# Kernel tuning notes

Hardware: AMD Instinct MI355X
Metric: run time of the kernel (lower is better)

## Reference

```python
import jax, jax.numpy as jnp
import numpy as np

DT = 0.02          # matches sdeint(dt=0.02)
N_STEPS = 50       # (times[-1]-times[0]) / DT with times = linspace(0, 1, 50)


def lipswish(x):
    # LipSwish activation: 0.909 * x * sigmoid(x)
    return 0.909 * x * jax.nn.sigmoid(x)


def mlp(y, ws, bs):
    # ws: [L, H, H], bs: [L, H]; LipSwish between layers, linear output
    L = ws.shape[0]
    for i in range(L):
        y = y @ ws[i] + bs[i]
        if i < L - 1:
            y = lipswish(y)
    return y


def setup_inputs() -> dict:
    key = jax.random.key(0)
    ks = jax.random.split(key, 12)
    B, T, D, H, FH, L = 1024, 50, 64, 1024, 128, 2

    def lin(k, fan_in, shape):
        return (jax.random.normal(k, shape, jnp.float32) / np.sqrt(fan_in)).astype(jnp.float32)

    return {
        "coeffs": jax.random.normal(ks[0], (B, T, D), jnp.float32),
        "times": jnp.linspace(0.0, 1.0, T).astype(jnp.float32),
        "dw": jax.random.normal(ks[1], (N_STEPS, B, H), jnp.float32),  # std-normal; scaled by sqrt(DT) inside
        # vector field: drift f and diagonal diffusion g, each a 2-layer MLP H->H
        "f_ws": lin(ks[2], H, (L, H, H)),
        "f_bs": jnp.zeros((L, H), jnp.float32),
        "g_ws": lin(ks[3], H, (L, H, H)),
        "g_bs": jnp.zeros((L, H), jnp.float32),
        # decoder / embedding layers
        "initial_w": lin(ks[4], D, (D, H)),
        "initial_b": jnp.zeros((H,), jnp.float32),
        "lin_in_w": lin(ks[5], H, (H, FH)),
        "lin_in_b": jnp.zeros((FH,), jnp.float32),
        "emb_w": lin(ks[6], 2 * FH, (2 * FH, H)),
        "emb_b": jnp.zeros((H,), jnp.float32),
        "samp_w": lin(ks[7], H, (H, FH)),
        "samp_b": jnp.zeros((FH,), jnp.float32),
    }


def reference(coeffs, times, dw, f_ws, f_bs, g_ws, g_bs,
              initial_w, initial_b, lin_in_w, lin_in_b,
              emb_w, emb_b, samp_w, samp_b):
    B = coeffs.shape[0]
    FH = samp_w.shape[1]

    # X.evaluate(times) at the interpolation knots == coeffs; take first time point
    y0 = (coeffs @ initial_w + initial_b)[:, 0, :]  # [B, H]

    sqrt_dt = jnp.asarray(np.sqrt(DT), y0.dtype)

    # Euler-Maruyama: y_{k+1} = y_k + f(t,y)*dt + g(t,y)*dW_k  (diagonal noise)
    def step(y, dwk):
        drift = mlp(y, f_ws, f_bs)
        diff = mlp(y, g_ws, g_bs)
        y = y + drift * DT + diff * (dwk * sqrt_dt)
        return y, None

    z, _ = jax.lax.scan(step, y0, dw)  # z: [B, H] (z_t[-1])

    t = jnp.broadcast_to(jnp.linspace(0.0, 1.0, FH, dtype=z.dtype), (B, FH))
    z = jax.nn.relu(z @ lin_in_w + lin_in_b)                      # [B, FH]
    z = jax.nn.relu(jnp.concatenate([z, t], axis=-1) @ emb_w + emb_b)  # [B, H]
    return z @ samp_w + samp_b                                    # [B, FH]
```

## Files before the change

kernel.cpp:

```cpp
#include <hip/hip_runtime.h>
#include <math.h>

typedef _Float16 f16;
typedef _Float16 f16x8 __attribute__((ext_vector_type(8)));
typedef float f32x4 __attribute__((ext_vector_type(4)));

#define BATCH   1024
#define HID     1024
#define DIN     64
#define TKNOTS  50
#define FHID    128
#define NSTEPS  50
#define DT_C      0.02f
#define SQRT_DT_C 0.1414213562373095f
#define LO_SCALE  2048.0f
#define INV_LO    4.8828125e-4f

__device__ __forceinline__ void gload16(const f16* g, const f16* l) {
  __builtin_amdgcn_global_load_lds((const __attribute__((address_space(1))) unsigned int*)g,
                                   (__attribute__((address_space(3))) unsigned int*)l, 16, 0, 0);
}

__device__ __forceinline__ void split_f32(float x, f16& hi, f16& lo) {
  hi = (f16)x;
  lo = (f16)((x - (float)hi) * LO_SCALE);
}

template<int MODE>
__global__ __launch_bounds__(256) void gemm3_k(
    const f16* __restrict__ Ah, const f16* __restrict__ Al, int lda, int aoff,
    const f16* __restrict__ Bh, const f16* __restrict__ Bl,
    const float* __restrict__ bias0, const float* __restrict__ bias1,
    float* __restrict__ Cf, f16* __restrict__ Ch, f16* __restrict__ Cl)
{
  __shared__ __align__(16) char smem[32768];

  const int tid = threadIdx.x;

  const int bid = blockIdx.x;
  const int r   = ((bid & 7) << 6) | (bid >> 3);
  const int m0  = (r & 15) << 6;
  const int n0  = (r >> 4) << 6;

  const f16* Ah_p = Ah + (n0 >= HID ? aoff : 0);
  const f16* Al_p = Al + (n0 >= HID ? aoff : 0);

  const int sr = tid >> 2;
  const int sc = (((tid & 3) << 4) ^ (((sr >> 1) & 3) << 4)) >> 1;
  const f16* gAh = Ah_p + (size_t)(m0 + sr) * lda + sc;
  const f16* gAl = Al_p + (size_t)(m0 + sr) * lda + sc;
  const f16* gBh = Bh   + (size_t)(n0 + sr) * HID + sc;
  const f16* gBl = Bl   + (size_t)(n0 + sr) * HID + sc;

  const int lane = tid & 63;
  const int wid  = tid >> 6;
  const int wm   = wid >> 1;
  const int wn   = wid & 1;
  const int fr   = lane & 15;
  const int fg   = lane >> 4;
  const int sig  = ((fr >> 1) & 3) << 4;
  const int kb   = (fg << 4) ^ sig;
  const int ra0  = (wm * 32 + fr) * 64;
  const int ra1  = ra0 + 16 * 64;
  const int rb0  = (wn * 32 + fr) * 64;
  const int rb1  = rb0 + 16 * 64;

  f32x4 acc1[2][2] = {};
  f32x4 acc2[2][2] = {};

  {
    char* db = smem + (tid << 4);
    gload16(gAh, (const f16*)(db));
    gload16(gAl, (const f16*)(db + 4096));
    gload16(gBh, (const f16*)(db + 8192));
    gload16(gBl, (const f16*)(db + 12288));
  }
  __syncthreads();

  int cur = 0;
  for (int kt = 0; kt < HID / 32; ++kt) {
    if (kt < HID / 32 - 1) {
      const int ko = (kt + 1) << 5;
      char* db = smem + ((cur ^ 1) * 16384) + (tid << 4);
      gload16(gAh + ko, (const f16*)(db));
      gload16(gAl + ko, (const f16*)(db + 4096));
      gload16(gBh + ko, (const f16*)(db + 8192));
      gload16(gBl + ko, (const f16*)(db + 12288));
    }

    const char* cb = smem + cur * 16384;
    f16x8 ah0 = *(const f16x8*)(cb + ra0 + kb);
    f16x8 ah1 = *(const f16x8*)(cb + ra1 + kb);
    f16x8 al0 = *(const f16x8*)(cb + 4096 + ra0 + kb);
    f16x8 al1 = *(const f16x8*)(cb + 4096 + ra1 + kb);
    f16x8 bh0 = *(const f16x8*)(cb + 8192 + rb0 + kb);
    f16x8 bh1 = *(const f16x8*)(cb + 8192 + rb1 + kb);
    f16x8 bl0 = *(const f16x8*)(cb + 12288 + rb0 + kb);
    f16x8 bl1 = *(const f16x8*)(cb + 12288 + rb1 + kb);

    acc1[0][0] = __builtin_amdgcn_mfma_f32_16x16x32_f16(ah0, bh0, acc1[0][0], 0, 0, 0);
    acc1[0][1] = __builtin_amdgcn_mfma_f32_16x16x32_f16(ah0, bh1, acc1[0][1], 0, 0, 0);
    acc1[1][0] = __builtin_amdgcn_mfma_f32_16x16x32_f16(ah1, bh0, acc1[1][0], 0, 0, 0);
    acc1[1][1] = __builtin_amdgcn_mfma_f32_16x16x32_f16(ah1, bh1, acc1[1][1], 0, 0, 0);
    acc2[0][0] = __builtin_amdgcn_mfma_f32_16x16x32_f16(ah0, bl0, acc2[0][0], 0, 0, 0);
    acc2[0][1] = __builtin_amdgcn_mfma_f32_16x16x32_f16(ah0, bl1, acc2[0][1], 0, 0, 0);
    acc2[1][0] = __builtin_amdgcn_mfma_f32_16x16x32_f16(ah1, bl0, acc2[1][0], 0, 0, 0);
    acc2[1][1] = __builtin_amdgcn_mfma_f32_16x16x32_f16(ah1, bl1, acc2[1][1], 0, 0, 0);
    acc2[0][0] = __builtin_amdgcn_mfma_f32_16x16x32_f16(al0, bh0, acc2[0][0], 0, 0, 0);
    acc2[0][1] = __builtin_amdgcn_mfma_f32_16x16x32_f16(al0, bh1, acc2[0][1], 0, 0, 0);
    acc2[1][0] = __builtin_amdgcn_mfma_f32_16x16x32_f16(al1, bh0, acc2[1][0], 0, 0, 0);
    acc2[1][1] = __builtin_amdgcn_mfma_f32_16x16x32_f16(al1, bh1, acc2[1][1], 0, 0, 0);

    __syncthreads();
    cur ^= 1;
  }

#pragma unroll
  for (int fm = 0; fm < 2; ++fm) {
#pragma unroll
    for (int fn = 0; fn < 2; ++fn) {
      const int row = m0 + wm * 32 + fm * 16 + fg * 4;
      const int col = n0 + wn * 32 + fn * 16 + fr;
      const float bs = (col < HID) ? bias0[col] : bias1[col - HID];
#pragma unroll
      for (int rr = 0; rr < 4; ++rr) {
        float v = acc1[fm][fn][rr] + acc2[fm][fn][rr] * INV_LO + bs;
        if (MODE == 1) {
          const float x = 0.909f * v / (1.0f + expf(-v));
          f16 hi, lo; split_f32(x, hi, lo);
          Ch[(size_t)(row + rr) * 2048 + col] = hi;
          Cl[(size_t)(row + rr) * 2048 + col] = lo;
        } else {
          Cf[(size_t)(row + rr) * 2048 + col] = v;
        }
      }
    }
  }
}

__global__ __launch_bounds__(256) void split_transpose_k(
    const float* __restrict__ f_ws, const float* __restrict__ g_ws,
    f16* __restrict__ Bt0h, f16* __restrict__ Bt0l,
    f16* __restrict__ Bt1h, f16* __restrict__ Bt1l)
{
  __shared__ float t[32][33];
  const int z = blockIdx.z;
  const float* src = (z & 1) ? g_ws : f_ws;
  if (z >= 2) src += (size_t)HID * HID;
  f16* dh = (z >= 2) ? Bt1h : Bt0h;
  f16* dl = (z >= 2) ? Bt1l : Bt0l;
  const int nb = (z & 1) ? HID : 0;

  const int tx = threadIdx.x;
  const int ty = threadIdx.y;
  const int k0 = blockIdx.y * 32;
  const int n0 = blockIdx.x * 32;
#pragma unroll
  for (int i = 0; i < 4; ++i)
    t[ty + i * 8][tx] = src[(size_t)(k0 + ty + i * 8) * HID + n0 + tx];
  __syncthreads();
#pragma unroll
  for (int i = 0; i < 4; ++i) {
    const int n = n0 + ty + i * 8;
    const int k = k0 + tx;
    const float v = t[tx][ty + i * 8];
    f16 hi, lo; split_f32(v, hi, lo);
    dh[(size_t)(nb + n) * HID + k] = hi;
    dl[(size_t)(nb + n) * HID + k] = lo;
  }
}

__global__ __launch_bounds__(256) void y0_k(
    const float* __restrict__ coeffs, const float* __restrict__ w,
    const float* __restrict__ b, float* __restrict__ y,
    f16* __restrict__ yh, f16* __restrict__ yl)
{
  __shared__ float c[DIN];
  const int bi = blockIdx.x;
  if (threadIdx.x < DIN) c[threadIdx.x] = coeffs[(size_t)bi * (TKNOTS * DIN) + threadIdx.x];
  __syncthreads();
#pragma unroll
  for (int rr = 0; rr < 4; ++rr) {
    const int j = threadIdx.x + rr * 256;
    float s = b[j];
#pragma unroll 8
    for (int d = 0; d < DIN; ++d) s = fmaf(c[d], w[(size_t)d * HID + j], s);
    y[(size_t)bi * HID + j] = s;
    f16 hi, lo; split_f32(s, hi, lo);
    yh[(size_t)bi * HID + j] = hi;
    yl[(size_t)bi * HID + j] = lo;
  }
}

__global__ __launch_bounds__(256) void update_y_k(
    float* __restrict__ y, f16* __restrict__ yh, f16* __restrict__ yl,
    const float* __restrict__ dd, const float* __restrict__ dwk)
{
  const int i   = blockIdx.x * 256 + threadIdx.x;
  const int row = i >> 8;
  const int c4  = (i & 255) << 2;
  float4 yv = *(float4*)(y + (size_t)row * HID + c4);
  const float4 dr = *(const float4*)(dd + (size_t)row * 2048 + c4);
  const float4 df = *(const float4*)(dd + (size_t)row * 2048 + HID + c4);
  const float4 wv = *(const float4*)(dwk + (size_t)row * HID + c4);
  yv.x = fmaf(DT_C, dr.x, fmaf(SQRT_DT_C * wv.x, df.x, yv.x));
  yv.y = fmaf(DT_C, dr.y, fmaf(SQRT_DT_C * wv.y, df.y, yv.y));
  yv.z = fmaf(DT_C, dr.z, fmaf(SQRT_DT_C * wv.z, df.z, yv.z));
  yv.w = fmaf(DT_C, dr.w, fmaf(SQRT_DT_C * wv.w, df.w, yv.w));
  *(float4*)(y + (size_t)row * HID + c4) = yv;
  const float vals[4] = {yv.x, yv.y, yv.z, yv.w};
#pragma unroll
  for (int t = 0; t < 4; ++t) {
    f16 hi, lo; split_f32(vals[t], hi, lo);
    yh[(size_t)row * HID + c4 + t] = hi;
    yl[(size_t)row * HID + c4 + t] = lo;
  }
}

#define BM 64
#define BN 64
#define BK 32
#define MODE_LIN  0
#define MODE_RELU 2

__global__ __launch_bounds__(256) void gemm_k(
    const float* __restrict__ A, int lda,
    const float* __restrict__ B0, int ldb,
    const float* __restrict__ bias0,
    float* __restrict__ C, int ldc, int K, int mode)
{
  __shared__ float As[BK][BM];
  __shared__ float Bs[BK][BN];
  const int t  = threadIdx.x;
  const int m0 = blockIdx.y * BM;
  const int n0 = blockIdx.x * BN;
  const int ar = t >> 3, ac = (t & 7) << 2;
  const int br = t >> 4, bc = (t & 15) << 2;
  const int i0 = (t >> 4) << 2, j0 = (t & 15) << 2;
  float acc[4][4];
#pragma unroll
  for (int rr = 0; rr < 4; ++rr)
#pragma unroll
    for (int c = 0; c < 4; ++c) acc[rr][c] = 0.0f;

  for (int k0 = 0; k0 < K; k0 += BK) {
    const float4 a0 = *(const float4*)(A + (size_t)(m0 + ar)      * lda + k0 + ac);
    const float4 a1 = *(const float4*)(A + (size_t)(m0 + ar + 32) * lda + k0 + ac);
    const float4 b0 = *(const float4*)(B0 + (size_t)(k0 + br)      * ldb + n0 + bc);
    const float4 b1 = *(const float4*)(B0 + (size_t)(k0 + br + 16) * ldb + n0 + bc);
    __syncthreads();
    As[ac + 0][ar] = a0.x; As[ac + 1][ar] = a0.y; As[ac + 2][ar] = a0.z; As[ac + 3][ar] = a0.w;
    As[ac + 0][ar + 32] = a1.x; As[ac + 1][ar + 32] = a1.y;
    As[ac + 2][ar + 32] = a1.z; As[ac + 3][ar + 32] = a1.w;
    *(float4*)&Bs[br][bc] = b0;
    *(float4*)&Bs[br + 16][bc] = b1;
    __syncthreads();
#pragma unroll
    for (int kk = 0; kk < BK; ++kk) {
      const float4 av = *(const float4*)&As[kk][i0];
      const float4 bv = *(const float4*)&Bs[kk][j0];
      const float a_[4] = {av.x, av.y, av.z, av.w};
      const float b_[4] = {bv.x, bv.y, bv.z, bv.w};
#pragma unroll
      for (int rr = 0; rr < 4; ++rr)
#pragma unroll
        for (int c = 0; c < 4; ++c)
          acc[rr][c] = fmaf(a_[rr], b_[c], acc[rr][c]);
    }
  }
#pragma unroll
  for (int rr = 0; rr < 4; ++rr) {
    float4 v; float* vp = &v.x;
#pragma unroll
    for (int c = 0; c < 4; ++c) {
      float x = acc[rr][c] + bias0[n0 + j0 + c];
      if (mode == MODE_RELU) x = fmaxf(x, 0.0f);
      vp[c] = x;
    }
    *(float4*)(C + (size_t)(m0 + i0 + rr) * ldc + n0 + j0) = v;
  }
}

__global__ __launch_bounds__(256) void tvec_k(
    const float* __restrict__ emb_w, const float* __restrict__ emb_b,
    float* __restrict__ tv)
{
  const int j = blockIdx.x * 256 + threadIdx.x;
  float s = emb_b[j];
#pragma unroll 8
  for (int k = 0; k < FHID; ++k)
    s = fmaf((float)k * (1.0f / 127.0f), emb_w[(size_t)(FHID + k) * HID + j], s);
  tv[j] = s;
}

extern "C" void kernel_launch(void* const* d_in, const int* in_sizes, int n_in,
                              void* d_out, int out_size, void* d_ws, size_t ws_size,
                              hipStream_t stream) {
  const float* coeffs    = (const float*)d_in[0];
  const float* dw        = (const float*)d_in[2];
  const float* f_ws      = (const float*)d_in[3];
  const float* f_bs      = (const float*)d_in[4];
  const float* g_ws      = (const float*)d_in[5];
  const float* g_bs      = (const float*)d_in[6];
  const float* initial_w = (const float*)d_in[7];
  const float* initial_b = (const float*)d_in[8];
  const float* lin_in_w  = (const float*)d_in[9];
  const float* lin_in_b  = (const float*)d_in[10];
  const float* emb_w     = (const float*)d_in[11];
  const float* emb_b     = (const float*)d_in[12];
  const float* samp_w    = (const float*)d_in[13];
  const float* samp_b    = (const float*)d_in[14];
  float* out = (float*)d_out;

  char* ws = (char*)d_ws;
  f16*   Bt0h = (f16*)(ws);
  f16*   Bt0l = (f16*)(ws + (4u << 20));
  f16*   Bt1h = (f16*)(ws + (8u << 20));
  f16*   Bt1l = (f16*)(ws + (12u << 20));
  f16*   yh   = (f16*)(ws + (16u << 20));
  f16*   yl   = (f16*)(ws + (18u << 20));
  f16*   hh   = (f16*)(ws + (20u << 20));
  f16*   hl   = (f16*)(ws + (24u << 20));
  float* y    = (float*)(ws + (28u << 20));
  float* dd   = (float*)(ws + (32u << 20));
  float* z1   = (float*)(ws + (40u << 20));
  float* z2   = (float*)(ws + (41u << 20));
  float* tv   = (float*)(ws + (45u << 20));

  split_transpose_k<<<dim3(HID / 32, HID / 32, 4), dim3(32, 8), 0, stream>>>(
      f_ws, g_ws, Bt0h, Bt0l, Bt1h, Bt1l);

  y0_k<<<BATCH, 256, 0, stream>>>(coeffs, initial_w, initial_b, y, yh, yl);

  for (int k = 0; k < NSTEPS; ++k) {
    gemm3_k<1><<<512, 256, 0, stream>>>(
        yh, yl, HID, 0, Bt0h, Bt0l, f_bs, g_bs, nullptr, hh, hl);
    gemm3_k<0><<<512, 256, 0, stream>>>(
        hh, hl, 2048, HID, Bt1h, Bt1l, f_bs + HID, g_bs + HID, dd, nullptr, nullptr);
    update_y_k<<<(BATCH * HID / 4) / 256, 256, 0, stream>>>(
        y, yh, yl, dd, dw + (size_t)k * BATCH * HID);
  }

  gemm_k<<<dim3(FHID / BN, BATCH / BM), 256, 0, stream>>>(
      y, HID, lin_in_w, FHID, lin_in_b, z1, FHID, HID, MODE_RELU);
  tvec_k<<<HID / 256, 256, 0, stream>>>(emb_w, emb_b, tv);
  gemm_k<<<dim3(HID / BN, BATCH / BM), 256, 0, stream>>>(
      z1, FHID, emb_w, HID, tv, z2, HID, FHID, MODE_RELU);
  gemm_k<<<dim3(FHID / BN, BATCH / BM), 256, 0, stream>>>(
      z2, HID, samp_w, FHID, samp_b, out, FHID, HID, MODE_LIN);
}
```

Measured before the change: 2.736 ms.

## Fuse second-layer GEMM with Euler-Maruyama update and triple-buffer first GEMM

The second-layer GEMM is restructured so each block computes matching drift and diffusion column tiles. Diffusion results are exchanged through shared memory and the y update is applied in the epilogue. This removes the separate update kernel and the round trip of the dd buffer through global memory. The first-layer GEMM moves to a three-stage LDS pipeline with explicit vmcnt waits and a single barrier per k-step, at the cost of more shared memory per block and therefore possibly lower occupancy.

```diff
diff --git a/kernel.cpp b/kernel.cpp
--- a/kernel.cpp
+++ b/kernel.cpp
@@ -26,77 +26,65 @@
   lo = (f16)((x - (float)hi) * LO_SCALE);
 }
 
-template<int MODE>
-__global__ __launch_bounds__(256) void gemm3_k(
-    const f16* __restrict__ Ah, const f16* __restrict__ Al, int lda, int aoff,
+__global__ __launch_bounds__(256) void g1_k(
+    const f16* __restrict__ Ah, const f16* __restrict__ Al,
     const f16* __restrict__ Bh, const f16* __restrict__ Bl,
     const float* __restrict__ bias0, const float* __restrict__ bias1,
-    float* __restrict__ Cf, f16* __restrict__ Ch, f16* __restrict__ Cl)
-{
-  __shared__ __align__(16) char smem[32768];
+    f16* __restrict__ Ch, f16* __restrict__ Cl)
+{
+  __shared__ __align__(16) char smem[49152];
 
   const int tid = threadIdx.x;
-
   const int bid = blockIdx.x;
   const int r   = ((bid & 7) << 6) | (bid >> 3);
   const int m0  = (r & 15) << 6;
   const int n0  = (r >> 4) << 6;
 
-  const f16* Ah_p = Ah + (n0 >= HID ? aoff : 0);
-  const f16* Al_p = Al + (n0 >= HID ? aoff : 0);
-
   const int sr = tid >> 2;
   const int sc = (((tid & 3) << 4) ^ (((sr >> 1) & 3) << 4)) >> 1;
-  const f16* gAh = Ah_p + (size_t)(m0 + sr) * lda + sc;
-  const f16* gAl = Al_p + (size_t)(m0 + sr) * lda + sc;
-  const f16* gBh = Bh   + (size_t)(n0 + sr) * HID + sc;
-  const f16* gBl = Bl   + (size_t)(n0 + sr) * HID + sc;
-
-  const int lane = tid & 63;
-  const int wid  = tid >> 6;
-  const int wm   = wid >> 1;
-  const int wn   = wid & 1;
-  const int fr   = lane & 15;
-  const int fg   = lane >> 4;
-  const int sig  = ((fr >> 1) & 3) << 4;
-  const int kb   = (fg << 4) ^ sig;
-  const int ra0  = (wm * 32 + fr) * 64;
-  const int ra1  = ra0 + 16 * 64;
-  const int rb0  = (wn * 32 + fr) * 64;
-  const int rb1  = rb0 + 16 * 64;
-
-  f32x4 acc1[2][2] = {};
-  f32x4 acc2[2][2] = {};
-
-  {
-    char* db = smem + (tid << 4);
-    gload16(gAh, (const f16*)(db));
-    gload16(gAl, (const f16*)(db + 4096));
-    gload16(gBh, (const f16*)(db + 8192));
-    gload16(gBl, (const f16*)(db + 12288));
-  }
-  __syncthreads();
-
-  int cur = 0;
-  for (int kt = 0; kt < HID / 32; ++kt) {
-    if (kt < HID / 32 - 1) {
-      const int ko = (kt + 1) << 5;
-      char* db = smem + ((cur ^ 1) * 16384) + (tid << 4);
-      gload16(gAh + ko, (const f16*)(db));
-      gload16(gAl + ko, (const f16*)(db + 4096));
-      gload16(gBh + ko, (const f16*)(db + 8192));
-      gload16(gBl + ko, (const f16*)(db + 12288));
-    }
-
-    const char* cb = smem + cur * 16384;
-    f16x8 ah0 = *(const f16x8*)(cb + ra0 + kb);
-    f16x8 ah1 = *(const f16x8*)(cb + ra1 + kb);
-    f16x8 al0 = *(const f16x8*)(cb + 4096 + ra0 + kb);
-    f16x8 al1 = *(const f16x8*)(cb + 4096 + ra1 + kb);
-    f16x8 bh0 = *(const f16x8*)(cb + 8192 + rb0 + kb);
-    f16x8 bh1 = *(const f16x8*)(cb + 8192 + rb1 + kb);
-    f16x8 bl0 = *(const f16x8*)(cb + 12288 + rb0 + kb);
-    f16x8 bl1 = *(const f16x8*)(cb + 12288 + rb1 + kb);
+  const f16* gAh = Ah + (size_t)(m0 + sr) * HID + sc;
+  const f16* gAl = Al + (size_t)(m0 + sr) * HID + sc;
+  const f16* gBh = Bh + (size_t)(n0 + sr) * HID + sc;
+  const f16* gBl = Bl + (size_t)(n0 + sr) * HID + sc;
+
+  const int lane = tid & 63, wid = tid >> 6;
+  const int wm = wid >> 1, wn = wid & 1;
+  const int fr = lane & 15, fg = lane >> 4;
+  const int kb = (fg << 4) ^ (((fr >> 1) & 3) << 4);
+  const int ra0 = (wm * 32 + fr) * 64 + kb, ra1 = ra0 + 1024;
+  const int rb0 = (wn * 32 + fr) * 64 + kb, rb1 = rb0 + 1024;
+
+  f32x4 acc1[2][2] = {}, acc2[2][2] = {};
+
+  auto stage = [&](int kt, int b) {
+    const int ko = kt << 5;
+    char* db = smem + b * 16384 + (tid << 4);
+    gload16(gAh + ko, (const f16*)db);
+    gload16(gAl + ko, (const f16*)(db + 4096));
+    gload16(gBh + ko, (const f16*)(db + 8192));
+    gload16(gBl + ko, (const f16*)(db + 12288));
+  };
+
+  stage(0, 0);
+  stage(1, 1);
+
+  int bsel = 0;
+  for (int kt = 0; kt < 32; ++kt) {
+    if (kt < 31) asm volatile("s_waitcnt vmcnt(4)" ::: "memory");
+    else         asm volatile("s_waitcnt vmcnt(0)" ::: "memory");
+    __builtin_amdgcn_s_barrier();
+    __builtin_amdgcn_sched_barrier(0);
+    if (kt + 2 < 32) { int nb = bsel + 2; if (nb >= 3) nb -= 3; stage(kt + 2, nb); }
+
+    const char* cb = smem + bsel * 16384;
+    f16x8 ah0 = *(const f16x8*)(cb + ra0);
+    f16x8 ah1 = *(const f16x8*)(cb + ra1);
+    f16x8 al0 = *(const f16x8*)(cb + 4096 + ra0);
+    f16x8 al1 = *(const f16x8*)(cb + 4096 + ra1);
+    f16x8 bh0 = *(const f16x8*)(cb + 8192 + rb0);
+    f16x8 bh1 = *(const f16x8*)(cb + 8192 + rb1);
+    f16x8 bl0 = *(const f16x8*)(cb + 12288 + rb0);
+    f16x8 bl1 = *(const f16x8*)(cb + 12288 + rb1);
 
     acc1[0][0] = __builtin_amdgcn_mfma_f32_16x16x32_f16(ah0, bh0, acc1[0][0], 0, 0, 0);
     acc1[0][1] = __builtin_amdgcn_mfma_f32_16x16x32_f16(ah0, bh1, acc1[0][1], 0, 0, 0);
@@ -111,12 +99,11 @@
     acc2[1][0] = __builtin_amdgcn_mfma_f32_16x16x32_f16(al1, bh0, acc2[1][0], 0, 0, 0);
     acc2[1][1] = __builtin_amdgcn_mfma_f32_16x16x32_f16(al1, bh1, acc2[1][1], 0, 0, 0);
 
-    __syncthreads();
-    cur ^= 1;
-  }
-
-#pragma unroll
-  for (int fm = 0; fm < 2; ++fm) {
+    bsel = (bsel == 2) ? 0 : bsel + 1;
+  }
+
+#pragma unroll
+  for (int fm = 0; fm < 2; ++fm)
 #pragma unroll
     for (int fn = 0; fn < 2; ++fn) {
       const int row = m0 + wm * 32 + fm * 16 + fg * 4;
@@ -124,17 +111,136 @@
       const float bs = (col < HID) ? bias0[col] : bias1[col - HID];
 #pragma unroll
       for (int rr = 0; rr < 4; ++rr) {
-        float v = acc1[fm][fn][rr] + acc2[fm][fn][rr] * INV_LO + bs;
-        if (MODE == 1) {
-          const float x = 0.909f * v / (1.0f + expf(-v));
-          f16 hi, lo; split_f32(x, hi, lo);
-          Ch[(size_t)(row + rr) * 2048 + col] = hi;
-          Cl[(size_t)(row + rr) * 2048 + col] = lo;
-        } else {
-          Cf[(size_t)(row + rr) * 2048 + col] = v;
-        }
+        const float v = acc1[fm][fn][rr] + acc2[fm][fn][rr] * INV_LO + bs;
+        const float x = 0.909f * v / (1.0f + expf(-v));
+        f16 hi, lo; split_f32(x, hi, lo);
+        Ch[(size_t)(row + rr) * 2048 + col] = hi;
+        Cl[(size_t)(row + rr) * 2048 + col] = lo;
       }
     }
+}
+
+__global__ __launch_bounds__(256) void g2u_k(
+    const f16* __restrict__ hh_, const f16* __restrict__ hl_,
+    const f16* __restrict__ B1h, const f16* __restrict__ B1l,
+    const float* __restrict__ biasf, const float* __restrict__ biasg,
+    const float* __restrict__ dwk,
+    float* __restrict__ y, f16* __restrict__ yh, f16* __restrict__ yl)
+{
+  __shared__ __align__(16) char smem[49152];
+
+  const int tid = threadIdx.x;
+  const int bid = blockIdx.x;
+  const int r   = ((bid & 7) << 6) | (bid >> 3);
+  const int m0  = (r & 15) << 6;
+  const int n0  = (r >> 4) << 5;
+
+  const int sr = tid >> 2;
+  const int sc = (((tid & 3) << 4) ^ (((sr >> 1) & 3) << 4)) >> 1;
+  const f16* gAfh = hh_ + (size_t)(m0 + sr) * 2048 + sc;
+  const f16* gAfl = hl_ + (size_t)(m0 + sr) * 2048 + sc;
+  const f16* gAgh = gAfh + HID;
+  const f16* gAgl = gAfl + HID;
+  const int btid = tid & 127;
+  const int bsr = btid >> 2;
+  const int bsc = (((btid & 3) << 4) ^ (((bsr >> 1) & 3) << 4)) >> 1;
+  const f16* Bsel = (tid < 128) ? B1h : B1l;
+  const f16* gBf = Bsel + (size_t)(n0 + bsr) * HID + bsc;
+  const f16* gBg = Bsel + (size_t)(HID + n0 + bsr) * HID + bsc;
+  const int dBoff = 16384 + ((tid >> 7) << 11) + (btid << 4);
+
+  const int lane = tid & 63, wid = tid >> 6;
+  const int wm = wid & 1, func = wid >> 1;
+  const int fr = lane & 15, fg = lane >> 4;
+  const int kb = (fg << 4) ^ (((fr >> 1) & 3) << 4);
+  const int Ab = func << 13;
+  const int ra0 = Ab + (wm * 32 + fr) * 64 + kb, ra1 = ra0 + 1024;
+  const int Bb = 16384 + (func << 12);
+  const int rb0 = Bb + fr * 64 + kb, rb1 = rb0 + 1024;
+
+  f32x4 acc1[2][2] = {}, acc2[2][2] = {};
+
+  auto stage = [&](int kt, int b) {
+    const int ko = kt << 5;
+    char* db = smem + b * 24576;
+    char* da = db + (tid << 4);
+    gload16(gAfh + ko, (const f16*)da);
+    gload16(gAfl + ko, (const f16*)(da + 4096));
+    gload16(gAgh + ko, (const f16*)(da + 8192));
+    gload16(gAgl + ko, (const f16*)(da + 12288));
+    gload16(gBf + ko, (const f16*)(db + dBoff));
+    gload16(gBg + ko, (const f16*)(db + dBoff + 4096));
+  };
+
+  stage(0, 0);
+  __syncthreads();
+
+  int cur = 0;
+  for (int kt = 0; kt < 32; ++kt) {
+    if (kt < 31) stage(kt + 1, cur ^ 1);
+
+    const char* cb = smem + cur * 24576;
+    f16x8 ah0 = *(const f16x8*)(cb + ra0);
+    f16x8 ah1 = *(const f16x8*)(cb + ra1);
+    f16x8 al0 = *(const f16x8*)(cb + ra0 + 4096);
+    f16x8 al1 = *(const f16x8*)(cb + ra1 + 4096);
+    f16x8 bh0 = *(const f16x8*)(cb + rb0);
+    f16x8 bh1 = *(const f16x8*)(cb + rb1);
+    f16x8 bl0 = *(const f16x8*)(cb + rb0 + 2048);
+    f16x8 bl1 = *(const f16x8*)(cb + rb1 + 2048);
+
+    acc1[0][0] = __builtin_amdgcn_mfma_f32_16x16x32_f16(ah0, bh0, acc1[0][0], 0, 0, 0);
+    acc1[0][1] = __builtin_amdgcn_mfma_f32_16x16x32_f16(ah0, bh1, acc1[0][1], 0, 0, 0);
+    acc1[1][0] = __builtin_amdgcn_mfma_f32_16x16x32_f16(ah1, bh0, acc1[1][0], 0, 0, 0);
+    acc1[1][1] = __builtin_amdgcn_mfma_f32_16x16x32_f16(ah1, bh1, acc1[1][1], 0, 0, 0);
+    acc2[0][0] = __builtin_amdgcn_mfma_f32_16x16x32_f16(ah0, bl0, acc2[0][0], 0, 0, 0);
+    acc2[0][1] = __builtin_amdgcn_mfma_f32_16x16x32_f16(ah0, bl1, acc2[0][1], 0, 0, 0);
+    acc2[1][0] = __builtin_amdgcn_mfma_f32_16x16x32_f16(ah1, bl0, acc2[1][0], 0, 0, 0);
+    acc2[1][1] = __builtin_amdgcn_mfma_f32_16x16x32_f16(ah1, bl1, acc2[1][1], 0, 0, 0);
+    acc2[0][0] = __builtin_amdgcn_mfma_f32_16x16x32_f16(al0, bh0, acc2[0][0], 0, 0, 0);
+    acc2[0][1] = __builtin_amdgcn_mfma_f32_16x16x32_f16(al0, bh1, acc2[0][1], 0, 0, 0);
+    acc2[1][0] = __builtin_amdgcn_mfma_f32_16x16x32_f16(al1, bh0, acc2[1][0], 0, 0, 0);
+    acc2[1][1] = __builtin_amdgcn_mfma_f32_16x16x32_f16(al1, bh1, acc2[1][1], 0, 0, 0);
+
+    __syncthreads();
+    cur ^= 1;
+  }
+
+  float* ex = (float*)smem;
+  if (func == 1) {
+#pragma unroll
+    for (int fm = 0; fm < 2; ++fm)
+#pragma unroll
+      for (int fn = 0; fn < 2; ++fn)
+#pragma unroll
+        for (int rr = 0; rr < 4; ++rr) {
+          const int lr = fm * 16 + fg * 4 + rr;
+          const int lc = fn * 16 + fr;
+          const float v = acc1[fm][fn][rr] + acc2[fm][fn][rr] * INV_LO + biasg[n0 + lc];
+          ex[wm * 1024 + lr * 32 + lc] = v;
+        }
+  }
+  __syncthreads();
+  if (func == 0) {
+#pragma unroll
+    for (int fm = 0; fm < 2; ++fm)
+#pragma unroll
+      for (int fn = 0; fn < 2; ++fn)
+#pragma unroll
+        for (int rr = 0; rr < 4; ++rr) {
+          const int lr = fm * 16 + fg * 4 + rr;
+          const int lc = fn * 16 + fr;
+          const int row = m0 + wm * 32 + lr;
+          const int col = n0 + lc;
+          const float drift = acc1[fm][fn][rr] + acc2[fm][fn][rr] * INV_LO + biasf[col];
+          const float diff  = ex[wm * 1024 + lr * 32 + lc];
+          const size_t idx  = (size_t)row * HID + col;
+          const float yn = fmaf(DT_C, drift, fmaf(SQRT_DT_C * dwk[idx], diff, y[idx]));
+          y[idx] = yn;
+          f16 hi, lo; split_f32(yn, hi, lo);
+          yh[idx] = hi;
+          yl[idx] = lo;
+        }
   }
 }
 
@@ -151,10 +257,8 @@
   f16* dl = (z >= 2) ? Bt1l : Bt0l;
   const int nb = (z & 1) ? HID : 0;
 
-  const int tx = threadIdx.x;
-  const int ty = threadIdx.y;
-  const int k0 = blockIdx.y * 32;
-  const int n0 = blockIdx.x * 32;
+  const int tx = threadIdx.x, ty = threadIdx.y;
+  const int k0 = blockIdx.y * 32, n0 = blockIdx.x * 32;
 #pragma unroll
   for (int i = 0; i < 4; ++i)
     t[ty + i * 8][tx] = src[(size_t)(k0 + ty + i * 8) * HID + n0 + tx];
@@ -163,8 +267,7 @@
   for (int i = 0; i < 4; ++i) {
     const int n = n0 + ty + i * 8;
     const int k = k0 + tx;
-    const float v = t[tx][ty + i * 8];
-    f16 hi, lo; split_f32(v, hi, lo);
+    f16 hi, lo; split_f32(t[tx][ty + i * 8], hi, lo);
     dh[(size_t)(nb + n) * HID + k] = hi;
     dl[(size_t)(nb + n) * HID + k] = lo;
   }
@@ -189,31 +292,6 @@
     f16 hi, lo; split_f32(s, hi, lo);
     yh[(size_t)bi * HID + j] = hi;
     yl[(size_t)bi * HID + j] = lo;
-  }
-}
-
-__global__ __launch_bounds__(256) void update_y_k(
-    float* __restrict__ y, f16* __restrict__ yh, f16* __restrict__ yl,
-    const float* __restrict__ dd, const float* __restrict__ dwk)
-{
-  const int i   = blockIdx.x * 256 + threadIdx.x;
-  const int row = i >> 8;
-  const int c4  = (i & 255) << 2;
-  float4 yv = *(float4*)(y + (size_t)row * HID + c4);
-  const float4 dr = *(const float4*)(dd + (size_t)row * 2048 + c4);
-  const float4 df = *(const float4*)(dd + (size_t)row * 2048 + HID + c4);
-  const float4 wv = *(const float4*)(dwk + (size_t)row * HID + c4);
-  yv.x = fmaf(DT_C, dr.x, fmaf(SQRT_DT_C * wv.x, df.x, yv.x));
-  yv.y = fmaf(DT_C, dr.y, fmaf(SQRT_DT_C * wv.y, df.y, yv.y));
-  yv.z = fmaf(DT_C, dr.z, fmaf(SQRT_DT_C * wv.z, df.z, yv.z));
-  yv.w = fmaf(DT_C, dr.w, fmaf(SQRT_DT_C * wv.w, df.w, yv.w));
-  *(float4*)(y + (size_t)row * HID + c4) = yv;
-  const float vals[4] = {yv.x, yv.y, yv.z, yv.w};
-#pragma unroll
-  for (int t = 0; t < 4; ++t) {
-    f16 hi, lo; split_f32(vals[t], hi, lo);
-    yh[(size_t)row * HID + c4 + t] = hi;
-    yl[(size_t)row * HID + c4 + t] = lo;
   }
 }
 
@@ -322,10 +400,9 @@
   f16*   hh   = (f16*)(ws + (20u << 20));
   f16*   hl   = (f16*)(ws + (24u << 20));
   float* y    = (float*)(ws + (28u << 20));
-  float* dd   = (float*)(ws + (32u << 20));
-  float* z1   = (float*)(ws + (40u << 20));
-  float* z2   = (float*)(ws + (41u << 20));
-  float* tv   = (float*)(ws + (45u << 20));
+  float* z1   = (float*)(ws + (32u << 20));
+  float* z2   = (float*)(ws + (33u << 20));
+  float* tv   = (float*)(ws + (37u << 20));
 
   split_transpose_k<<<dim3(HID / 32, HID / 32, 4), dim3(32, 8), 0, stream>>>(
       f_ws, g_ws, Bt0h, Bt0l, Bt1h, Bt1l);
@@ -333,12 +410,9 @@
   y0_k<<<BATCH, 256, 0, stream>>>(coeffs, initial_w, initial_b, y, yh, yl);
 
   for (int k = 0; k < NSTEPS; ++k) {
-    gemm3_k<1><<<512, 256, 0, stream>>>(
-        yh, yl, HID, 0, Bt0h, Bt0l, f_bs, g_bs, nullptr, hh, hl);
-    gemm3_k<0><<<512, 256, 0, stream>>>(
-        hh, hl, 2048, HID, Bt1h, Bt1l, f_bs + HID, g_bs + HID, dd, nullptr, nullptr);
-    update_y_k<<<(BATCH * HID / 4) / 256, 256, 0, stream>>>(
-        y, yh, yl, dd, dw + (size_t)k * BATCH * HID);
+    g1_k<<<512, 256, 0, stream>>>(yh, yl, Bt0h, Bt0l, f_bs, g_bs, hh, hl);
+    g2u_k<<<512, 256, 0, stream>>>(hh, hl, Bt1h, Bt1l, f_bs + HID, g_bs + HID,
+                                   dw + (size_t)k * BATCH * HID, y, yh, yl);
   }
 
   gemm_k<<<dim3(FHID / BN, BATCH / BM), 256, 0, stream>>>(
```

Result: slower. 3.180 ms (+16.2%).
